# Optimization experiments

Hardware: AMD Instinct MI355X
Metric: run time of the kernel (lower is better)

The kernel has to match this reference:

```python
import jax, jax.numpy as jnp
from jax import lax
import numpy as np

VOCAB, EMB = 32000, 300
NF, FSIZES = 100, (3, 4, 5)
HID, OUT = 256, 32
B, T, L = 32, 64, 48


def setup_inputs() -> dict:
    key = jax.random.key(0)
    ks = jax.random.split(key, 16)
    inp = {}
    inp["dialogue"] = jax.random.randint(ks[0], (B, T, L), 0, VOCAB, dtype=jnp.int32)
    inp["emb"] = jax.random.normal(ks[1], (VOCAB, EMB), jnp.float32) * 0.1
    for j, fs in enumerate(FSIZES):
        inp[f"conv_w{fs}"] = jax.random.normal(ks[2 + j], (NF, EMB, fs), jnp.float32) * 0.05
        inp[f"conv_b{fs}"] = jnp.zeros((NF,), jnp.float32)
    D = NF * len(FSIZES)  # LSTM input size = 300
    for j, tag in enumerate(("f", "r")):
        inp[f"w_ih_{tag}"] = jax.random.normal(ks[5 + 2 * j], (4 * HID, D), jnp.float32) * 0.05
        inp[f"w_hh_{tag}"] = jax.random.normal(ks[6 + 2 * j], (4 * HID, HID), jnp.float32) * 0.05
        inp[f"b_ih_{tag}"] = jnp.zeros((4 * HID,), jnp.float32)
        inp[f"b_hh_{tag}"] = jnp.zeros((4 * HID,), jnp.float32)
    inp["head_w"] = jax.random.normal(ks[9], (OUT, 2 * HID), jnp.float32) * 0.05
    inp["head_b"] = jnp.zeros((OUT,), jnp.float32)
    return inp


def _lstm(x_tbd, w_ih, w_hh, b_ih, b_hh):
    # x_tbd: [T, B, D] -> hidden sequence [T, B, H]; torch gate order i,f,g,o
    H = w_hh.shape[1]
    Bsz = x_tbd.shape[1]
    # precompute input projections for all timesteps in one GEMM
    xg = jnp.einsum('tbd,gd->tbg', x_tbd, w_ih) + (b_ih + b_hh)

    def step(carry, xg_t):
        h, c = carry
        gates = xg_t + h @ w_hh.T
        i, f, g, o = jnp.split(gates, 4, axis=-1)
        c = jax.nn.sigmoid(f) * c + jax.nn.sigmoid(i) * jnp.tanh(g)
        h = jax.nn.sigmoid(o) * jnp.tanh(c)
        return (h, c), h

    h0 = jnp.zeros((Bsz, H), x_tbd.dtype)
    _, hs = lax.scan(step, (h0, h0), xg)
    return hs


def reference(dialogue, emb, conv_w3, conv_b3, conv_w4, conv_b4, conv_w5, conv_b5,
              w_ih_f, w_hh_f, b_ih_f, b_hh_f, w_ih_r, w_hh_r, b_ih_r, b_hh_r,
              head_w, head_b):
    Bd, Td, Ld = dialogue.shape
    x = emb[dialogue.reshape(Bd * Td, Ld)]      # [BT, L, E]
    x = x.transpose(0, 2, 1)                     # [BT, E, L] (NCH)
    feats = []
    for w, b in ((conv_w3, conv_b3), (conv_w4, conv_b4), (conv_w5, conv_b5)):
        # Conv2d(1,NF,(fs,E)) on [BT,1,L,E] == 1D valid conv over L with E in-channels
        y = lax.conv_general_dilated(x, w, (1,), 'VALID',
                                     dimension_numbers=('NCH', 'OIH', 'NCH'))
        y = jax.nn.relu(y + b[None, :, None])    # [BT, NF, L-fs+1]
        feats.append(jnp.max(y, axis=2))         # max_pool1d over full width
    r_in = jnp.concatenate(feats, axis=1).reshape(Bd, Td, -1)  # dropout = identity (eval)
    xt = r_in.transpose(1, 0, 2)                 # [T, B, D]
    hf = _lstm(xt, w_ih_f, w_hh_f, b_ih_f, b_hh_f)            # forward direction
    hr = _lstm(xt[::-1], w_ih_r, w_hh_r, b_ih_r, b_hh_r)[::-1]  # reverse direction
    h = jnp.concatenate([hf, hr], axis=-1).transpose(1, 0, 2)  # [B, T, 2H]
    return jax.nn.sigmoid(jnp.einsum('bth,oh->bto', h, head_w) + head_b)
```

## Files before the change

### kernel.cpp

```cpp
#include <hip/hip_runtime.h>
#include <math.h>

typedef unsigned short u16;
typedef unsigned int   u32;
typedef unsigned long long u64;
typedef float  v16f __attribute__((ext_vector_type(16)));
typedef short  v8s  __attribute__((ext_vector_type(8)));

__device__ __forceinline__ float sigf(float x) { return 1.0f / (1.0f + __expf(-x)); }
__device__ __forceinline__ float tanhfast(float x) { return 2.0f / (1.0f + __expf(-2.0f * x)) - 1.0f; }
__device__ __forceinline__ u16 f2bf(float f) {
    u32 x = __float_as_uint(f);
    u32 r = (x + 0x7fffu + ((x >> 16) & 1u)) >> 16;
    return (u16)r;
}

#define KE        19
#define SLAB      2048
#define G0_OFF    0
#define G1_OFF    (3 * KE * SLAB)
#define G2_OFF    (7 * KE * SLAB)
#define WKR_TOT   (12 * KE * SLAB)
#define XSTR      312

__global__ __launch_bounds__(256) void k_cprep(const float* __restrict__ w3,
                                               const float* __restrict__ w4,
                                               const float* __restrict__ w5,
                                               u16* __restrict__ wkr) {
    const int gid = blockIdx.x * 256 + threadIdx.x;
    int g, rem;
    if (gid < G1_OFF)      { g = 0; rem = gid; }
    else if (gid < G2_OFF) { g = 1; rem = gid - G1_OFF; }
    else                   { g = 2; rem = gid - G2_OFF; }
    const int fs = 3 + g;
    const int j  = rem & 7;
    const int q  = (rem >> 3) & 1;
    const int f  = (rem >> 4) & 127;
    const int t  = rem >> 11;
    const int ke = t % KE;
    const int kk = t / KE;
    const int e  = ke * 16 + q * 8 + j;
    float v = 0.0f;
    if (f < 100 && e < 300) {
        const float* w = (g == 0) ? w3 : (g == 1) ? w4 : w5;
        v = w[((size_t)f * 300 + e) * fs + kk];
    }
    wkr[gid] = f2bf(v);
}

__global__ __launch_bounds__(384) void k_conv_mfma(const int* __restrict__ dlg,
                                                   const float* __restrict__ emb,
                                                   const u16* __restrict__ wkr,
                                                   const float* __restrict__ b3,
                                                   const float* __restrict__ b4,
                                                   const float* __restrict__ b5,
                                                   float* __restrict__ feat) {
    __shared__ u16 xT[104 * XSTR];
    __shared__ int toks[96];
    const int u2  = blockIdx.x;
    const int tid = threadIdx.x;
    if (tid < 96) toks[tid] = dlg[u2 * 96 + tid];
    __syncthreads();
    for (int i = tid; i < 96 * 75; i += 384) {
        int t  = i / 75;
        int e4 = i - t * 75;
        int utt = (t >= 48);
        int row = utt * 52 + (t - utt * 48);
        float4 v = *(const float4*)(emb + (size_t)toks[t] * 300 + e4 * 4);
        uint2 o;
        o.x = (u32)f2bf(v.x) | ((u32)f2bf(v.y) << 16);
        o.y = (u32)f2bf(v.z) | ((u32)f2bf(v.w) << 16);
        *(uint2*)&xT[row * XSTR + e4 * 4] = o;
    }
    for (int i = tid; i < 8 * (XSTR / 2); i += 384) {
        int r = i / (XSTR / 2);
        int c = i - r * (XSTR / 2);
        int row = (r < 4) ? (48 + r) : (96 + r - 4);
        *(u32*)&xT[row * XSTR + c * 2] = 0;
    }
    __syncthreads();

    const int wv   = tid >> 6;
    const int lane = tid & 63;
    const int m    = lane & 31;
    const int q    = lane >> 5;

    int abase[3];
#pragma unroll
    for (int mt = 0; mt < 3; ++mt) {
        int r = mt * 32 + m;
        int utt = (r >= 48);
        int p = r - utt * 48;
        abase[mt] = (utt * 52 + p) * XSTR + q * 8;
    }

    int gA, ntA, gB, ntB, kkA, kkB;
    if (wv < 4) { gA = 0; ntA = wv; gB = 2; ntB = wv; kkA = 3; kkB = 5; }
    else        { gA = 1; ntA = (wv - 4) * 2; gB = 1; ntB = ntA + 1; kkA = 4; kkB = 4; }
    const int goffA = (gA == 0) ? G0_OFF : (gA == 1) ? G1_OFF : G2_OFF;
    const int goffB = (gB == 0) ? G0_OFF : (gB == 1) ? G1_OFF : G2_OFF;
    const u16* wA = wkr + goffA + ((ntA * 32 + m) * 2 + q) * 8;
    const u16* wB = wkr + goffB + ((ntB * 32 + m) * 2 + q) * 8;

    v16f accA[3], accB[3];
#pragma unroll
    for (int mt = 0; mt < 3; ++mt) {
#pragma unroll
        for (int r = 0; r < 16; ++r) { accA[mt][r] = 0.0f; accB[mt][r] = 0.0f; }
    }

    const int kmin = (kkA < kkB) ? kkA : kkB;
    const u16* pA = wA;
    const u16* pB = wB;
    v8s bfA = *(const v8s*)pA;
    v8s bfB = *(const v8s*)pB;
    for (int kk = 0; kk < kmin; ++kk) {
        const int xshift = kk * XSTR;
        for (int ke = 0; ke < KE; ++ke) {
            v8s cA = bfA, cB = bfB;
            pA += SLAB; pB += SLAB;
            bfA = *(const v8s*)pA;
            bfB = *(const v8s*)pB;
            const int xcol = xshift + ke * 16;
#pragma unroll
            for (int mt = 0; mt < 3; ++mt) {
                v8s af = *(const v8s*)&xT[abase[mt] + xcol];
                accA[mt] = __builtin_amdgcn_mfma_f32_32x32x16_bf16(af, cA, accA[mt], 0, 0, 0);
                accB[mt] = __builtin_amdgcn_mfma_f32_32x32x16_bf16(af, cB, accB[mt], 0, 0, 0);
            }
        }
    }
    for (int kk = kmin; kk < kkB; ++kk) {
        const int xshift = kk * XSTR;
        for (int ke = 0; ke < KE; ++ke) {
            v8s cB = bfB;
            pB += SLAB;
            bfB = *(const v8s*)pB;
            const int xcol = xshift + ke * 16;
#pragma unroll
            for (int mt = 0; mt < 3; ++mt) {
                v8s af = *(const v8s*)&xT[abase[mt] + xcol];
                accB[mt] = __builtin_amdgcn_mfma_f32_32x32x16_bf16(af, cB, accB[mt], 0, 0, 0);
            }
        }
    }

    const int PP[3] = {46, 45, 44};
#pragma unroll
    for (int which = 0; which < 2; ++which) {
        const int g  = which ? gB : gA;
        const int nt = which ? ntB : ntA;
        const v16f* acc = which ? accB : accA;
        const float* bg = (g == 0) ? b3 : (g == 1) ? b4 : b5;
        const int f = nt * 32 + m;
        const float bias = (f < 100) ? bg[f] : 0.0f;
        const int Pg = PP[g];
        float v0 = -1e30f, v1 = -1e30f;
#pragma unroll
        for (int mt = 0; mt < 3; ++mt) {
#pragma unroll
            for (int reg = 0; reg < 16; ++reg) {
                int row = (reg & 3) + 8 * (reg >> 2) + 4 * q;
                int r = mt * 32 + row;
                int utt = (r >= 48);
                int p = r - utt * 48;
                if (p < Pg) {
                    float val = acc[mt][reg] + bias;
                    if (utt) v1 = fmaxf(v1, val); else v0 = fmaxf(v0, val);
                }
            }
        }
        v0 = fmaxf(v0, __shfl_xor(v0, 32, 64));
        v1 = fmaxf(v1, __shfl_xor(v1, 32, 64));
        if (q == 0 && f < 100) {
            feat[((size_t)(u2 * 2 + 0)) * 300 + g * 100 + f] = fmaxf(0.0f, v0);
            feat[((size_t)(u2 * 2 + 1)) * 300 + g * 100 + f] = fmaxf(0.0f, v1);
        }
    }
}

__global__ __launch_bounds__(256) void k_xg(const float* __restrict__ feat,
                                            const float* __restrict__ wih_f, const float* __restrict__ bih_f,
                                            const float* __restrict__ bhh_f,
                                            const float* __restrict__ wih_r, const float* __restrict__ bih_r,
                                            const float* __restrict__ bhh_r,
                                            float* __restrict__ xgF) {
    __shared__ float fls[300 * 36];
    const int bx  = blockIdx.x;
    const int dir = bx >> 8;
    const int t   = (bx >> 2) & 63;
    const int gc  = bx & 3;
    const int tid = threadIdx.x;
    for (int i = tid; i < 32 * 300; i += 256) {
        int b = i / 300;
        int d = i - b * 300;
        fls[d * 36 + b] = feat[((size_t)b * 64 + t) * 300 + d];
    }
    __syncthreads();
    const int g = gc * 256 + tid;
    const float* wih = dir ? wih_r : wih_f;
    const float* bih = dir ? bih_r : bih_f;
    const float* bhh = dir ? bhh_r : bhh_f;
    const float* wr  = wih + (size_t)g * 300;
    const float bias = bih[g] + bhh[g];
    float acc[32];
#pragma unroll
    for (int b = 0; b < 32; ++b) acc[b] = 0.0f;
    for (int d = 0; d < 300; d += 4) {
        float4 wv = *(const float4*)(wr + d);
#pragma unroll
        for (int j = 0; j < 4; ++j) {
            float w = (j == 0) ? wv.x : (j == 1) ? wv.y : (j == 2) ? wv.z : wv.w;
            const float* r = &fls[(d + j) * 36];
#pragma unroll
            for (int bq = 0; bq < 8; ++bq) {
                float4 x = *(const float4*)(r + bq * 4);
                acc[bq * 4 + 0] = fmaf(w, x.x, acc[bq * 4 + 0]);
                acc[bq * 4 + 1] = fmaf(w, x.y, acc[bq * 4 + 1]);
                acc[bq * 4 + 2] = fmaf(w, x.z, acc[bq * 4 + 2]);
                acc[bq * 4 + 3] = fmaf(w, x.w, acc[bq * 4 + 3]);
            }
        }
    }
    const int jj      = tid;
    const int js      = jj >> 6;
    const int n_local = ((jj & 63) << 2) | gc;
    const int nt      = n_local >> 5;
    const int lane_lo = n_local & 31;
    float* base = xgF + (((size_t)(dir * 64 + t) * 32) + js * 8 + nt) * 1024;
#pragma unroll
    for (int b = 0; b < 32; ++b) {
        int q    = (b >> 2) & 1;
        int reg  = (b & 3) + ((b >> 3) << 2);
        base[reg * 64 + lane_lo + (q << 5)] = acc[b] + bias;
    }
}

__global__ __launch_bounds__(256) void k_prep3(const float* __restrict__ whh_f,
                                               const float* __restrict__ whh_r,
                                               u16* __restrict__ wpk3) {
    const int gid  = blockIdx.x * 256 + threadIdx.x;
    const int j    = gid & 7;
    const int lane = (gid >> 3) & 63;
    const int kt   = (gid >> 9) & 15;
    const int nt   = (gid >> 13) & 7;
    const int js   = (gid >> 16) & 3;
    const int dir  = (gid >> 18) & 1;
    const int n_local = nt * 32 + (lane & 31);
    const int jjl  = n_local >> 2;
    const int gate = n_local & 3;
    const int k    = kt * 16 + (lane >> 5) * 8 + j;
    const int row  = gate * 256 + js * 64 + jjl;
    const float* whh = dir ? whh_r : whh_f;
    wpk3[gid] = f2bf(whh[(size_t)row * 256 + k]);
}

__global__ __launch_bounds__(64) void k_init(u32* __restrict__ sent) {
    if (threadIdx.x < 8) sent[threadIdx.x] = 0u;
}

__global__ __launch_bounds__(512) void k_lstm3(const u16* __restrict__ wpk3,
                                               const float* __restrict__ xgF,
                                               u64* __restrict__ hx,
                                               u32* __restrict__ sent,
                                               float* __restrict__ hseq) {
    __shared__ u32   hbuf[32 * 132];
    __shared__ float gbuf[32 * 276];
    const int dir = blockIdx.x >> 2;
    const int js  = blockIdx.x & 3;
    const int tid = threadIdx.x;
    const int w   = tid >> 6;
    const int l   = tid & 63;
    const int m   = l & 31;
    const int q   = l >> 5;

    v8s Bf[16];
    {
        const u16* wb = wpk3 + ((((size_t)dir * 4 + js) * 8 + w) * 16) * 512 + (size_t)l * 8;
#pragma unroll
        for (int kt = 0; kt < 16; ++kt) Bf[kt] = *(const v8s*)(wb + kt * 512);
    }

    const int eb  = tid & 31;
    const int ejb = tid >> 5;
    float cst[4], hval[4];
#pragma unroll
    for (int c2 = 0; c2 < 4; ++c2) { cst[c2] = 0.0f; hval[c2] = 0.0f; }

    float* hout = hseq + (size_t)dir * 64 * 32 * 256;
    u64* hx_d   = hx + (size_t)dir * 2 * 2048;
    const int peer = (tid < 3) ? (dir * 4 + tid + (tid >= js ? 1 : 0)) : 0;

    for (int s = 0; s < 64; ++s) {
        const int t = dir ? (63 - s) : s;
        v16f acc;
        const float* xb = xgF + (((size_t)(dir * 64 + t) * 32) + js * 8 + w) * 1024 + l;
#pragma unroll
        for (int r = 0; r < 16; ++r) acc[r] = xb[r * 64];

        if (s > 0 && tid < 3) {
            u32 guard = 0;
            while (__hip_atomic_load(&sent[peer], __ATOMIC_RELAXED,
                                     __HIP_MEMORY_SCOPE_AGENT) < (u32)s) {
                __builtin_amdgcn_s_sleep(1);
                if (++guard > (1u << 25)) break;
            }
        }
        __syncthreads();

        if (s > 0) {
            const u64* hxs = hx_d + (size_t)(s & 1) * 2048;
#pragma unroll
            for (int i = 0; i < 3; ++i) {
                int flat = i * 512 + tid;
                int b    = flat / 48;
                int r    = flat - b * 48;
                int q64  = r + (r >= js * 16 ? 16 : 0);
                u64 v = __hip_atomic_load(&hxs[b * 64 + q64],
                                          __ATOMIC_RELAXED, __HIP_MEMORY_SCOPE_AGENT);
                *(u64*)&hbuf[b * 132 + q64 * 2] = v;
            }
        } else {
            for (int i = tid; i < 32 * 132; i += 512) hbuf[i] = 0u;
        }
        {
            u64 pk = (u64)f2bf(hval[0]) | ((u64)f2bf(hval[1]) << 16)
                   | ((u64)f2bf(hval[2]) << 32) | ((u64)f2bf(hval[3]) << 48);
            *(u64*)&hbuf[eb * 132 + (js * 16 + ejb) * 2] = pk;
        }
        __syncthreads();

#pragma unroll
        for (int kt = 0; kt < 16; ++kt) {
            v8s af = *(const v8s*)&hbuf[m * 132 + kt * 8 + q * 4];
            acc = __builtin_amdgcn_mfma_f32_32x32x16_bf16(af, Bf[kt], acc, 0, 0, 0);
        }

#pragma unroll
        for (int r = 0; r < 16; ++r) {
            int row = (r & 3) + 8 * (r >> 2) + 4 * q;
            gbuf[row * 276 + w * 32 + m] = acc[r];
        }
        __syncthreads();

        {
            const float* gb = &gbuf[eb * 276 + ejb * 16];
#pragma unroll
            for (int c2 = 0; c2 < 4; ++c2) {
                float4 gv = *(const float4*)(gb + c2 * 4);
                float i_ = sigf(gv.x), f_ = sigf(gv.y);
                float g_ = tanhfast(gv.z), o_ = sigf(gv.w);
                cst[c2] = f_ * cst[c2] + i_ * g_;
                hval[c2] = o_ * tanhfast(cst[c2]);
            }
        }
        {
            float4 hv4 = make_float4(hval[0], hval[1], hval[2], hval[3]);
            *(float4*)&hout[((size_t)t * 32 + eb) * 256 + js * 64 + ejb * 4] = hv4;
            u64 pk = (u64)f2bf(hval[0]) | ((u64)f2bf(hval[1]) << 16)
                   | ((u64)f2bf(hval[2]) << 32) | ((u64)f2bf(hval[3]) << 48);
            u64* hxn = hx_d + (size_t)((s + 1) & 1) * 2048;
            __hip_atomic_store(&hxn[eb * 64 + js * 16 + ejb], pk,
                               __ATOMIC_RELAXED, __HIP_MEMORY_SCOPE_AGENT);
        }
        __syncthreads();
        if (tid == 0) {
            __hip_atomic_store(&sent[dir * 4 + js], (u32)(s + 1),
                               __ATOMIC_RELAXED, __HIP_MEMORY_SCOPE_AGENT);
        }
    }
}

__global__ __launch_bounds__(256) void k_head(const float* __restrict__ hseq,
                                              const float* __restrict__ hw,
                                              const float* __restrict__ hb,
                                              float* __restrict__ out) {
    const int id = blockIdx.x * 256 + threadIdx.x;
    const int o  = id & 31;
    const int u  = id >> 5;
    const int b  = u >> 6, t = u & 63;
    const float* pf = hseq + ((size_t)t * 32 + b) * 256;
    const float* pr = hseq + (size_t)64 * 32 * 256 + ((size_t)t * 32 + b) * 256;
    const float* wo = hw + (size_t)o * 512;
    float acc = hb[o];
    for (int j = 0; j < 256; j += 4) {
        float4 wa = *(const float4*)(wo + j);
        float4 wb = *(const float4*)(wo + 256 + j);
        float4 fa = *(const float4*)(pf + j);
        float4 fb = *(const float4*)(pr + j);
        acc = fmaf(wa.x, fa.x, acc); acc = fmaf(wa.y, fa.y, acc);
        acc = fmaf(wa.z, fa.z, acc); acc = fmaf(wa.w, fa.w, acc);
        acc = fmaf(wb.x, fb.x, acc); acc = fmaf(wb.y, fb.y, acc);
        acc = fmaf(wb.z, fb.z, acc); acc = fmaf(wb.w, fb.w, acc);
    }
    out[id] = sigf(acc);
}

extern "C" void kernel_launch(void* const* d_in, const int* in_sizes, int n_in,
                              void* d_out, int out_size, void* d_ws, size_t ws_size,
                              hipStream_t stream) {
    const int*   dlg   = (const int*)d_in[0];
    const float* emb   = (const float*)d_in[1];
    const float* w3    = (const float*)d_in[2];  const float* b3    = (const float*)d_in[3];
    const float* w4    = (const float*)d_in[4];  const float* b4    = (const float*)d_in[5];
    const float* w5    = (const float*)d_in[6];  const float* b5    = (const float*)d_in[7];
    const float* wih_f = (const float*)d_in[8];  const float* whh_f = (const float*)d_in[9];
    const float* bih_f = (const float*)d_in[10]; const float* bhh_f = (const float*)d_in[11];
    const float* wih_r = (const float*)d_in[12]; const float* whh_r = (const float*)d_in[13];
    const float* bih_r = (const float*)d_in[14]; const float* bhh_r = (const float*)d_in[15];
    const float* hw    = (const float*)d_in[16]; const float* hb    = (const float*)d_in[17];
    float* out = (float*)d_out;

    float* f     = (float*)d_ws;
    float* feat  = f;
    float* xgF   = f + 614400;
    float* hseq  = f + 4808704;
    u16*   wkr   = (u16*)(f + 5857280);
    u16*   wpk3  = (u16*)(f + 6090752);
    u64*   hx    = (u64*)(f + 6352896);
    u32*   sent  = (u32*)(f + 6369280);

    hipLaunchKernelGGL(k_init, dim3(1), dim3(64), 0, stream, sent);
    hipLaunchKernelGGL(k_cprep, dim3(WKR_TOT / 256), dim3(256), 0, stream,
                       w3, w4, w5, wkr);
    hipLaunchKernelGGL(k_prep3, dim3(2048), dim3(256), 0, stream,
                       whh_f, whh_r, wpk3);
    hipLaunchKernelGGL(k_conv_mfma, dim3(1024), dim3(384), 0, stream,
                       dlg, emb, wkr, b3, b4, b5, feat);
    hipLaunchKernelGGL(k_xg, dim3(512), dim3(256), 0, stream,
                       feat, wih_f, bih_f, bhh_f, wih_r, bih_r, bhh_r, xgF);
    hipLaunchKernelGGL(k_lstm3, dim3(8), dim3(512), 0, stream,
                       wpk3, xgF, hx, sent, hseq);
    hipLaunchKernelGGL(k_head, dim3(256), dim3(256), 0, stream,
                       hseq, hw, hb, out);
}
```

Measured before the change: 568.5 us.

## Replace per-block sentinel flags with step-tagged hidden-state records polled directly

Drops the separate per-block step counter and its spin-then-barrier handshake in the recurrent LSTM kernel. Each thread now writes its packed bf16 hidden values together with a step tag as one 16-byte record using system-coherent stores. Consumers poll those records directly with coherent 16-byte loads until the tag matches, which removes one barrier and the flag round trip on every timestep. In exchange the hidden-state exchange buffer doubles in size, every thread spins instead of three, and the timeout guard is shorter.

```diff
diff --git a/kernel.cpp b/kernel.cpp
--- a/kernel.cpp
+++ b/kernel.cpp
@@ -6,6 +6,7 @@
 typedef unsigned long long u64;
 typedef float  v16f __attribute__((ext_vector_type(16)));
 typedef short  v8s  __attribute__((ext_vector_type(8)));
+typedef unsigned int v4u __attribute__((ext_vector_type(4)));
 
 __device__ __forceinline__ float sigf(float x) { return 1.0f / (1.0f + __expf(-x)); }
 __device__ __forceinline__ float tanhfast(float x) { return 2.0f / (1.0f + __expf(-2.0f * x)) - 1.0f; }
@@ -14,6 +15,20 @@
     u32 r = (x + 0x7fffu + ((x >> 16) & 1u)) >> 16;
     return (u16)r;
 }
+
+#define LD3SYS(v0, v1, v2, p0, p1, p2)                                        \
+    asm volatile("global_load_dwordx4 %0, %3, off sc0 sc1\n\t"                \
+                 "global_load_dwordx4 %1, %4, off sc0 sc1\n\t"                \
+                 "global_load_dwordx4 %2, %5, off sc0 sc1\n\t"                \
+                 "s_waitcnt vmcnt(0)"                                         \
+                 : "=&v"(v0), "=&v"(v1), "=&v"(v2)                            \
+                 : "v"(p0), "v"(p1), "v"(p2)                                  \
+                 : "memory")
+
+#define ST16SYS(p, v)                                                         \
+    asm volatile("global_store_dwordx4 %0, %1, off sc0 sc1\n\t"               \
+                 "s_waitcnt vmcnt(0)"                                         \
+                 :: "v"(p), "v"(v) : "memory")
 
 #define KE        19
 #define SLAB      2048
@@ -255,14 +270,15 @@
     wpk3[gid] = f2bf(whh[(size_t)row * 256 + k]);
 }
 
-__global__ __launch_bounds__(64) void k_init(u32* __restrict__ sent) {
-    if (threadIdx.x < 8) sent[threadIdx.x] = 0u;
+__global__ __launch_bounds__(256) void k_init(v4u* __restrict__ hxrec) {
+    const int id = blockIdx.x * 256 + threadIdx.x;
+    v4u z; z[0] = 0u; z[1] = 0u; z[2] = 0u; z[3] = 0u;
+    hxrec[id] = z;
 }
 
 __global__ __launch_bounds__(512) void k_lstm3(const u16* __restrict__ wpk3,
                                                const float* __restrict__ xgF,
-                                               u64* __restrict__ hx,
-                                               u32* __restrict__ sent,
+                                               u32* __restrict__ hxrec,
                                                float* __restrict__ hseq) {
     __shared__ u32   hbuf[32 * 132];
     __shared__ float gbuf[32 * 276];
@@ -288,8 +304,21 @@
     for (int c2 = 0; c2 < 4; ++c2) { cst[c2] = 0.0f; hval[c2] = 0.0f; }
 
     float* hout = hseq + (size_t)dir * 64 * 32 * 256;
-    u64* hx_d   = hx + (size_t)dir * 2 * 2048;
-    const int peer = (tid < 3) ? (dir * 4 + tid + (tid >= js ? 1 : 0)) : 0;
+    u32* hx_d   = hxrec + (size_t)dir * 2 * 2048 * 4;
+    const u32* hx0 = hx_d;
+    const u32* hx1 = hx_d + 2048 * 4;
+
+    int roff[3], hoff[3];
+#pragma unroll
+    for (int i = 0; i < 3; ++i) {
+        int flat = i * 512 + tid;
+        int b    = flat / 48;
+        int r    = flat - b * 48;
+        int q64  = r + (r >= js * 16 ? 16 : 0);
+        roff[i]  = (b * 64 + q64) * 4;
+        hoff[i]  = b * 132 + q64 * 2;
+    }
+    const int woff = (eb * 64 + js * 16 + ejb) * 4;
 
     for (int s = 0; s < 64; ++s) {
         const int t = dir ? (63 - s) : s;
@@ -298,28 +327,22 @@
 #pragma unroll
         for (int r = 0; r < 16; ++r) acc[r] = xb[r * 64];
 
-        if (s > 0 && tid < 3) {
+        if (s > 0) {
+            const u32* hxs = (s & 1) ? hx1 : hx0;
+            const u32* p0 = hxs + roff[0];
+            const u32* p1 = hxs + roff[1];
+            const u32* p2 = hxs + roff[2];
+            v4u v0, v1, v2;
+            LD3SYS(v0, v1, v2, p0, p1, p2);
+            const u32 ts = (u32)s;
             u32 guard = 0;
-            while (__hip_atomic_load(&sent[peer], __ATOMIC_RELAXED,
-                                     __HIP_MEMORY_SCOPE_AGENT) < (u32)s) {
-                __builtin_amdgcn_s_sleep(1);
-                if (++guard > (1u << 25)) break;
-            }
-        }
-        __syncthreads();
-
-        if (s > 0) {
-            const u64* hxs = hx_d + (size_t)(s & 1) * 2048;
-#pragma unroll
-            for (int i = 0; i < 3; ++i) {
-                int flat = i * 512 + tid;
-                int b    = flat / 48;
-                int r    = flat - b * 48;
-                int q64  = r + (r >= js * 16 ? 16 : 0);
-                u64 v = __hip_atomic_load(&hxs[b * 64 + q64],
-                                          __ATOMIC_RELAXED, __HIP_MEMORY_SCOPE_AGENT);
-                *(u64*)&hbuf[b * 132 + q64 * 2] = v;
-            }
+            while (v0[2] != ts || v1[2] != ts || v2[2] != ts) {
+                if (++guard > (1u << 22)) break;
+                LD3SYS(v0, v1, v2, p0, p1, p2);
+            }
+            *(u64*)&hbuf[hoff[0]] = (u64)v0[0] | ((u64)v0[1] << 32);
+            *(u64*)&hbuf[hoff[1]] = (u64)v1[0] | ((u64)v1[1] << 32);
+            *(u64*)&hbuf[hoff[2]] = (u64)v2[0] | ((u64)v2[1] << 32);
         } else {
             for (int i = tid; i < 32 * 132; i += 512) hbuf[i] = 0u;
         }
@@ -359,14 +382,13 @@
             *(float4*)&hout[((size_t)t * 32 + eb) * 256 + js * 64 + ejb * 4] = hv4;
             u64 pk = (u64)f2bf(hval[0]) | ((u64)f2bf(hval[1]) << 16)
                    | ((u64)f2bf(hval[2]) << 32) | ((u64)f2bf(hval[3]) << 48);
-            u64* hxn = hx_d + (size_t)((s + 1) & 1) * 2048;
-            __hip_atomic_store(&hxn[eb * 64 + js * 16 + ejb], pk,
-                               __ATOMIC_RELAXED, __HIP_MEMORY_SCOPE_AGENT);
-        }
-        __syncthreads();
-        if (tid == 0) {
-            __hip_atomic_store(&sent[dir * 4 + js], (u32)(s + 1),
-                               __ATOMIC_RELAXED, __HIP_MEMORY_SCOPE_AGENT);
+            v4u rec;
+            rec[0] = (u32)pk;
+            rec[1] = (u32)(pk >> 32);
+            rec[2] = (u32)(s + 1);
+            rec[3] = 0u;
+            u32* pw = (u32*)(((s & 1) ? hx0 : hx1) + woff);
+            ST16SYS(pw, rec);
         }
     }
 }
@@ -417,10 +439,9 @@
     float* hseq  = f + 4808704;
     u16*   wkr   = (u16*)(f + 5857280);
     u16*   wpk3  = (u16*)(f + 6090752);
-    u64*   hx    = (u64*)(f + 6352896);
-    u32*   sent  = (u32*)(f + 6369280);
-
-    hipLaunchKernelGGL(k_init, dim3(1), dim3(64), 0, stream, sent);
+    u32*   hxrec = (u32*)(f + 6352896);
+
+    hipLaunchKernelGGL(k_init, dim3(32), dim3(256), 0, stream, (v4u*)hxrec);
     hipLaunchKernelGGL(k_cprep, dim3(WKR_TOT / 256), dim3(256), 0, stream,
                        w3, w4, w5, wkr);
     hipLaunchKernelGGL(k_prep3, dim3(2048), dim3(256), 0, stream,
@@ -430,7 +451,7 @@
     hipLaunchKernelGGL(k_xg, dim3(512), dim3(256), 0, stream,
                        feat, wih_f, bih_f, bhh_f, wih_r, bih_r, bhh_r, xgF);
     hipLaunchKernelGGL(k_lstm3, dim3(8), dim3(512), 0, stream,
-                       wpk3, xgF, hx, sent, hseq);
+                       wpk3, xgF, hxrec, hseq);
     hipLaunchKernelGGL(k_head, dim3(256), dim3(256), 0, stream,
                        hseq, hw, hb, out);
 }
```

New measurement: 552.9 us. -2.7%, faster.

## Split LSTM recurrence by batch instead of hidden units to drop inter-block sync

Applied to the files above, without the earlier changes.

The recurrent LSTM kernel now splits work across the four blocks per direction by batch group (8 sequences each) instead of by hidden-unit slice. Each block computes all 256 hidden units for its own batch rows, so the cross-block hidden-state exchange through global memory and the spin-wait flags are no longer needed. In exchange, each block streams the full recurrent weight matrix from global/L2 every timestep instead of keeping a slice in registers. Only a quarter of each MFMA's rows carry useful data, and the init kernel is dropped.

```diff
diff --git a/kernel.cpp b/kernel.cpp
--- a/kernel.cpp
+++ b/kernel.cpp
@@ -255,118 +255,76 @@
     wpk3[gid] = f2bf(whh[(size_t)row * 256 + k]);
 }
 
-__global__ __launch_bounds__(64) void k_init(u32* __restrict__ sent) {
-    if (threadIdx.x < 8) sent[threadIdx.x] = 0u;
-}
-
 __global__ __launch_bounds__(512) void k_lstm3(const u16* __restrict__ wpk3,
                                                const float* __restrict__ xgF,
-                                               u64* __restrict__ hx,
-                                               u32* __restrict__ sent,
                                                float* __restrict__ hseq) {
     __shared__ u32   hbuf[32 * 132];
-    __shared__ float gbuf[32 * 276];
+    __shared__ float slab[8 * 320];
     const int dir = blockIdx.x >> 2;
-    const int js  = blockIdx.x & 3;
+    const int bg  = blockIdx.x & 3;
     const int tid = threadIdx.x;
     const int w   = tid >> 6;
     const int l   = tid & 63;
     const int m   = l & 31;
     const int q   = l >> 5;
 
-    v8s Bf[16];
-    {
-        const u16* wb = wpk3 + ((((size_t)dir * 4 + js) * 8 + w) * 16) * 512 + (size_t)l * 8;
-#pragma unroll
-        for (int kt = 0; kt < 16; ++kt) Bf[kt] = *(const v8s*)(wb + kt * 512);
-    }
-
-    const int eb  = tid & 31;
-    const int ejb = tid >> 5;
+    for (int i = tid; i < 32 * 132; i += 512) hbuf[i] = 0u;
+
+    float* sl = &slab[w * 320];
+    const int bl = l >> 3;
+    const int jj = l & 7;
+    u16* hb16 = (u16*)hbuf;
+
     float cst[4], hval[4];
 #pragma unroll
     for (int c2 = 0; c2 < 4; ++c2) { cst[c2] = 0.0f; hval[c2] = 0.0f; }
 
     float* hout = hseq + (size_t)dir * 64 * 32 * 256;
-    u64* hx_d   = hx + (size_t)dir * 2 * 2048;
-    const int peer = (tid < 3) ? (dir * 4 + tid + (tid >= js ? 1 : 0)) : 0;
 
     for (int s = 0; s < 64; ++s) {
         const int t = dir ? (63 - s) : s;
-        v16f acc;
-        const float* xb = xgF + (((size_t)(dir * 64 + t) * 32) + js * 8 + w) * 1024 + l;
-#pragma unroll
-        for (int r = 0; r < 16; ++r) acc[r] = xb[r * 64];
-
-        if (s > 0 && tid < 3) {
-            u32 guard = 0;
-            while (__hip_atomic_load(&sent[peer], __ATOMIC_RELAXED,
-                                     __HIP_MEMORY_SCOPE_AGENT) < (u32)s) {
-                __builtin_amdgcn_s_sleep(1);
-                if (++guard > (1u << 25)) break;
-            }
-        }
         __syncthreads();
 
-        if (s > 0) {
-            const u64* hxs = hx_d + (size_t)(s & 1) * 2048;
-#pragma unroll
-            for (int i = 0; i < 3; ++i) {
-                int flat = i * 512 + tid;
-                int b    = flat / 48;
-                int r    = flat - b * 48;
-                int q64  = r + (r >= js * 16 ? 16 : 0);
-                u64 v = __hip_atomic_load(&hxs[b * 64 + q64],
-                                          __ATOMIC_RELAXED, __HIP_MEMORY_SCOPE_AGENT);
-                *(u64*)&hbuf[b * 132 + q64 * 2] = v;
-            }
-        } else {
-            for (int i = tid; i < 32 * 132; i += 512) hbuf[i] = 0u;
-        }
-        {
-            u64 pk = (u64)f2bf(hval[0]) | ((u64)f2bf(hval[1]) << 16)
-                   | ((u64)f2bf(hval[2]) << 32) | ((u64)f2bf(hval[3]) << 48);
-            *(u64*)&hbuf[eb * 132 + (js * 16 + ejb) * 2] = pk;
-        }
+        v8s af[16];
+#pragma unroll
+        for (int kt = 0; kt < 16; ++kt)
+            af[kt] = *(const v8s*)&hbuf[m * 132 + kt * 8 + q * 4];
+
+#pragma unroll
+        for (int c2 = 0; c2 < 4; ++c2) {
+            const u16* wb = wpk3 + ((((size_t)dir * 4 + c2) * 8 + w) * 16) * 512 + (size_t)l * 8;
+            v8s Bfc[16];
+#pragma unroll
+            for (int kt = 0; kt < 16; ++kt) Bfc[kt] = *(const v8s*)(wb + kt * 512);
+
+            const float* xb = xgF + (((size_t)(dir * 64 + t) * 32) + c2 * 8 + w) * 1024
+                            + bg * 256 + q * 32 + m;
+            v16f acc;
+#pragma unroll
+            for (int r = 0; r < 4; ++r) acc[r] = xb[r * 64];
+#pragma unroll
+            for (int r = 4; r < 16; ++r) acc[r] = 0.0f;
+
+#pragma unroll
+            for (int kt = 0; kt < 16; ++kt)
+                acc = __builtin_amdgcn_mfma_f32_32x32x16_bf16(af[kt], Bfc[kt], acc, 0, 0, 0);
+
+#pragma unroll
+            for (int r = 0; r < 4; ++r) sl[(r + 4 * q) * 40 + m] = acc[r];
+            asm volatile("s_waitcnt lgkmcnt(0)" ::: "memory");
+            float4 gv = *(const float4*)&sl[bl * 40 + jj * 4];
+            float i_ = sigf(gv.x), f_ = sigf(gv.y);
+            float g_ = tanhfast(gv.z), o_ = sigf(gv.w);
+            cst[c2]  = f_ * cst[c2] + i_ * g_;
+            hval[c2] = o_ * tanhfast(cst[c2]);
+        }
+
         __syncthreads();
-
-#pragma unroll
-        for (int kt = 0; kt < 16; ++kt) {
-            v8s af = *(const v8s*)&hbuf[m * 132 + kt * 8 + q * 4];
-            acc = __builtin_amdgcn_mfma_f32_32x32x16_bf16(af, Bf[kt], acc, 0, 0, 0);
-        }
-
-#pragma unroll
-        for (int r = 0; r < 16; ++r) {
-            int row = (r & 3) + 8 * (r >> 2) + 4 * q;
-            gbuf[row * 276 + w * 32 + m] = acc[r];
-        }
-        __syncthreads();
-
-        {
-            const float* gb = &gbuf[eb * 276 + ejb * 16];
-#pragma unroll
-            for (int c2 = 0; c2 < 4; ++c2) {
-                float4 gv = *(const float4*)(gb + c2 * 4);
-                float i_ = sigf(gv.x), f_ = sigf(gv.y);
-                float g_ = tanhfast(gv.z), o_ = sigf(gv.w);
-                cst[c2] = f_ * cst[c2] + i_ * g_;
-                hval[c2] = o_ * tanhfast(cst[c2]);
-            }
-        }
-        {
-            float4 hv4 = make_float4(hval[0], hval[1], hval[2], hval[3]);
-            *(float4*)&hout[((size_t)t * 32 + eb) * 256 + js * 64 + ejb * 4] = hv4;
-            u64 pk = (u64)f2bf(hval[0]) | ((u64)f2bf(hval[1]) << 16)
-                   | ((u64)f2bf(hval[2]) << 32) | ((u64)f2bf(hval[3]) << 48);
-            u64* hxn = hx_d + (size_t)((s + 1) & 1) * 2048;
-            __hip_atomic_store(&hxn[eb * 64 + js * 16 + ejb], pk,
-                               __ATOMIC_RELAXED, __HIP_MEMORY_SCOPE_AGENT);
-        }
-        __syncthreads();
-        if (tid == 0) {
-            __hip_atomic_store(&sent[dir * 4 + js], (u32)(s + 1),
-                               __ATOMIC_RELAXED, __HIP_MEMORY_SCOPE_AGENT);
+#pragma unroll
+        for (int c2 = 0; c2 < 4; ++c2) {
+            const int j = c2 * 64 + 8 * w + jj;
+            hb16[bl * 264 + j] = f2bf(hval[c2]);
+            hout[((size_t)t * 32 + bg * 8 + bl) * 256 + j] = hval[c2];
         }
     }
 }
@@ -417,10 +375,7 @@
     float* hseq  = f + 4808704;
     u16*   wkr   = (u16*)(f + 5857280);
     u16*   wpk3  = (u16*)(f + 6090752);
-    u64*   hx    = (u64*)(f + 6352896);
-    u32*   sent  = (u32*)(f + 6369280);
-
-    hipLaunchKernelGGL(k_init, dim3(1), dim3(64), 0, stream, sent);
+
     hipLaunchKernelGGL(k_cprep, dim3(WKR_TOT / 256), dim3(256), 0, stream,
                        w3, w4, w5, wkr);
     hipLaunchKernelGGL(k_prep3, dim3(2048), dim3(256), 0, stream,
@@ -430,7 +385,7 @@
     hipLaunchKernelGGL(k_xg, dim3(512), dim3(256), 0, stream,
                        feat, wih_f, bih_f, bhh_f, wih_r, bih_r, bhh_r, xgF);
     hipLaunchKernelGGL(k_lstm3, dim3(8), dim3(512), 0, stream,
-                       wpk3, xgF, hx, sent, hseq);
+                       wpk3, xgF, hseq);
     hipLaunchKernelGGL(k_head, dim3(256), dim3(256), 0, stream,
                        hseq, hw, hb, out);
 }
```

New measurement: 796.6 us. 1.4x slower.
